# Kernel tuning notes

Measured on AMD Instinct MI355X. Metric: run time of the kernel, lower is better.

The kernel has to match this reference:

```python
import jax, jax.numpy as jnp
import numpy as np

B, SQ, D = 1, 2048, 1024          # batch, seq, hidden
H, DH = 16, 64                    # heads, head dim
NC = 4096                         # intermediate_size (num_class of LSH layer)
K, L = 8, 16                      # hash funcs per table, num tables
NBUCKETS = 2 ** K
TPP = 1024                        # num_tokens_per_pass
S = 1024                          # fixed LSH sample budget per chunk
P = 64                            # pos/neg set size for triplet loss
MARGIN = 0.5
EPS = 1e-12


def setup_inputs() -> dict:
    key = jax.random.key(0)
    ks = jax.random.split(key, 12)
    def n(k, shape, s=0.02):
        return jax.random.normal(k, shape, dtype=jnp.float32) * s
    return {
        "hidden_states": jax.random.normal(ks[0], (B, SQ, D), dtype=jnp.float32),
        "attention_mask": jnp.ones((B, SQ), jnp.float32),
        "ln1_g": jnp.ones((D,), jnp.float32), "ln1_b": jnp.zeros((D,), jnp.float32),
        "Wq": n(ks[1], (D, D)), "bq": jnp.zeros((D,), jnp.float32),
        "Wk": n(ks[2], (D, D)), "bk": jnp.zeros((D,), jnp.float32),
        "Wv": n(ks[3], (D, D)), "bv": jnp.zeros((D,), jnp.float32),
        "Wo": n(ks[4], (D, D)), "bo": jnp.zeros((D,), jnp.float32),
        "ln2_g": jnp.ones((D,), jnp.float32), "ln2_b": jnp.zeros((D,), jnp.float32),
        "W1": n(ks[5], (NC, D), 0.03), "b1": jnp.zeros((NC,), jnp.float32),
        "Whash": jax.random.normal(ks[6], (L, K, D), dtype=jnp.float32),
        "W2": n(ks[7], (NC, D), 0.0156), "b2": jnp.zeros((D,), jnp.float32),
    }


def _layernorm(x, g, b):
    m = x.mean(-1, keepdims=True)
    v = x.var(-1, keepdims=True)
    return (x - m) / jnp.sqrt(v + EPS) * g + b


def _forward(hidden_states, attention_mask, ln1_g, ln1_b, Wq, bq, Wk, bk, Wv, bv,
             Wo, bo, ln2_g, ln2_b, W1, b1, Whash, W2, b2):
    # ---------------- Attention (pre-LN, residual) ----------------
    x = _layernorm(hidden_states, ln1_g, ln1_b)
    def heads(w, bb):
        y = jnp.einsum('bsd,ed->bse', x, w) + bb
        return y.reshape(B, SQ, H, DH).transpose(0, 2, 1, 3)  # [B,H,S,DH]
    q, k, v = heads(Wq, bq), heads(Wk, bk), heads(Wv, bv)
    scale = DH ** 0.25                              # sqrt(sqrt(head_size))
    mask = -1000.0 * (1.0 - attention_mask)[:, None, None, :]
    scores = jnp.einsum('bhqd,bhkd->bhqk', q / scale, k / scale) + mask
    probs = jax.nn.softmax(scores, axis=-1)
    ctx = jnp.einsum('bhqk,bhkd->bhqd', probs, v)
    ctx = ctx.transpose(0, 2, 1, 3).reshape(B, SQ, D)
    attn_out = jnp.einsum('bsd,ed->bse', ctx, Wo) + bo + hidden_states

    # ---------------- SlideFFN: LSH-routed sparse FFN ----------------
    flat = attn_out.reshape(B * SQ, D)
    normed = _layernorm(flat, ln2_g, ln2_b)
    pow2 = (2 ** jnp.arange(K)).astype(jnp.int32)
    # rehash(): SimHash codes of all NC first-layer neurons, per table. [L, NC]
    code_n = (((jnp.einsum('lkd,nd->lnk', Whash, W1) > 0).astype(jnp.int32)) * pow2).sum(-1)

    def chunk_fn(h):                                 # h: [TPP, D]
        proj_t = jnp.einsum('lkd,td->ltk', Whash, h)              # [L,T,K]
        code_t = (((proj_t > 0).astype(jnp.int32)) * pow2).sum(-1)  # [L,T]
        # bucket histogram of token codes per table
        hist = jax.vmap(lambda c: jnp.zeros(NBUCKETS, jnp.float32).at[c].add(1.0))(code_t)
        # collision score per neuron: tokens sharing its bucket, summed over tables
        score = jnp.take_along_axis(hist, code_n, axis=1).sum(0)   # [NC]
        _, sids = jax.lax.top_k(score, S)                          # fixed sample budget
        w1s, b1s = W1[sids], b1[sids]                              # gather sampled rows
        logits = h @ w1s.T + b1s                                   # [T,S] sample_logits
        acts = jax.nn.gelu(logits, approximate=False)
        out = acts @ W2[sids] + b2                                 # [T,D]
        # triplet loss: hash agreement should track logit ranking
        proj_ns = jnp.einsum('lkd,sd->lsk', Whash, w1s)
        agree = jnp.einsum('ltk,lsk->ts', jnp.tanh(proj_t), jnp.tanh(proj_ns)) / (L * K)
        pos_idx = jax.lax.top_k(logits, P)[1]
        neg_idx = jax.lax.top_k(-logits, P)[1]
        a_pos = jnp.take_along_axis(agree, pos_idx, axis=1).mean(-1)
        a_neg = jnp.take_along_axis(agree, neg_idx, axis=1).mean(-1)
        triplet = jax.nn.relu(a_neg - a_pos + MARGIN).mean()
        return out, triplet

    C = (B * SQ) // TPP
    outs, trips = jax.vmap(chunk_fn)(normed.reshape(C, TPP, D))
    ffn_out = outs.reshape(B, SQ, D)
    layer_output = ffn_out + attn_out
    return layer_output, trips.mean()


def reference(hidden_states, attention_mask, ln1_g, ln1_b, Wq, bq, Wk, bk, Wv, bv,
              Wo, bo, ln2_g, ln2_b, W1, b1, Whash, W2, b2):
    return _forward(hidden_states, attention_mask, ln1_g, ln1_b, Wq, bq, Wk, bk,
                    Wv, bv, Wo, bo, ln2_g, ln2_b, W1, b1, Whash, W2, b2)
```

## Files before the change

### kernel.cpp

```cpp
#include <hip/hip_runtime.h>
#include <hip/hip_bf16.h>
#include <math.h>

typedef __hip_bfloat16 bf16;
__device__ __forceinline__ float b2f(bf16 x) { return __bfloat162float(x); }
__device__ __forceinline__ unsigned fkey(float f) {
    unsigned u = __float_as_uint(f);
    return (u & 0x80000000u) ? ~u : (u | 0x80000000u);
}

#define LN_EPS 1e-12f
#define NEG_INF (-3.0e38f)

__global__ __launch_bounds__(256)
void copy_int_kernel(const int* __restrict__ src, int* __restrict__ dst, int n)
{
    int i = blockIdx.x * 256 + threadIdx.x;
    if (i < n) dst[i] = src[i];
}

__global__ __launch_bounds__(256)
void ln_kernel(const float* __restrict__ in, const float* __restrict__ g,
               const float* __restrict__ b, float* __restrict__ out)
{
    const int D = 1024;
    int row = blockIdx.x, tid = threadIdx.x;
    size_t base = (size_t)row * D + tid * 4;
    float x[4];
    #pragma unroll
    for (int i = 0; i < 4; ++i) x[i] = in[base + i];
    double s  = (double)x[0] + x[1] + x[2] + x[3];
    double sq = (double)x[0]*x[0] + (double)x[1]*x[1] + (double)x[2]*x[2] + (double)x[3]*x[3];
    __shared__ double rs[256], rq[256];
    rs[tid] = s; rq[tid] = sq;
    __syncthreads();
    for (int o = 128; o > 0; o >>= 1) {
        if (tid < o) { rs[tid] += rs[tid + o]; rq[tid] += rq[tid + o]; }
        __syncthreads();
    }
    double mean = rs[0] * (1.0 / D);
    double var  = rq[0] * (1.0 / D) - mean * mean;
    double inv  = rsqrt(var + (double)LN_EPS);
    #pragma unroll
    for (int i = 0; i < 4; ++i) {
        int col = tid * 4 + i;
        out[base + i] = (float)(((double)x[i] - mean) * inv * (double)g[col] + (double)b[col]);
    }
}

#define BM 64
#define BN 64
#define BK 16
template<typename ACC>
__global__ __launch_bounds__(256)
void gemm_nt_t(const float* __restrict__ A, int lda,
               const float* __restrict__ B, int ldb,
               const int* __restrict__ gatherB,
               const float* __restrict__ bias,
               const float* __restrict__ residual,
               void* __restrict__ out_, int oBf, int ldc, int mode,
               int M, int N, int Kd)
{
    __shared__ __align__(16) float As[BK][BM + 4];
    __shared__ __align__(16) float Bs[BK][BN + 4];
    int tid = threadIdx.x;
    int bm = blockIdx.y * BM, bn = blockIdx.x * BN;
    int lm  = tid >> 2;
    int lk4 = (tid & 3) * 4;
    int tm = (tid >> 4) * 4, tn = (tid & 15) * 4;
    ACC acc[4][4] = {};
    for (int k0 = 0; k0 < Kd; k0 += BK) {
        {
            const float* p = A + (size_t)(bm + lm) * lda + k0 + lk4;
            #pragma unroll
            for (int i = 0; i < 4; ++i) As[lk4 + i][lm] = p[i];
        }
        {
            int r = bn + lm;
            if (gatherB) r = gatherB[r] & 4095;
            const float* p = B + (size_t)r * ldb + k0 + lk4;
            #pragma unroll
            for (int i = 0; i < 4; ++i) Bs[lk4 + i][lm] = p[i];
        }
        __syncthreads();
        #pragma unroll
        for (int k = 0; k < BK; ++k) {
            float4 av = *(const float4*)&As[k][tm];
            float4 bw = *(const float4*)&Bs[k][tn];
            float avx[4] = {av.x, av.y, av.z, av.w};
            float bwx[4] = {bw.x, bw.y, bw.z, bw.w};
            #pragma unroll
            for (int i = 0; i < 4; ++i)
                #pragma unroll
                for (int j = 0; j < 4; ++j)
                    acc[i][j] += (ACC)avx[i] * (ACC)bwx[j];
        }
        __syncthreads();
    }
    #pragma unroll
    for (int i = 0; i < 4; ++i) {
        int m = bm + tm + i;
        #pragma unroll
        for (int j = 0; j < 4; ++j) {
            int n = bn + tn + j;
            ACC v = acc[i][j];
            if (bias) { int bi2 = gatherB ? (gatherB[n] & 4095) : n; v += (ACC)bias[bi2]; }
            if (residual) v += (ACC)residual[(size_t)m * ldc + n];
            size_t idx;
            if (mode == 0)      idx = (size_t)m * ldc + n;
            else if (mode == 1) idx = (size_t)(n >> 6) * ((size_t)M * 64) + (size_t)m * 64 + (n & 63);
            else                idx = (size_t)(n >> 3) * ((size_t)M * 8) + (size_t)m * 8 + (n & 7);
            if (oBf) ((bf16*)out_)[idx] = __float2bfloat16((float)v);
            else     ((float*)out_)[idx] = (float)v;
        }
    }
}

__global__ __launch_bounds__(256)
void qkv_kernel(const float* __restrict__ A,
                const float* __restrict__ Wq, const float* __restrict__ Wk, const float* __restrict__ Wv,
                const float* __restrict__ bq, const float* __restrict__ bk, const float* __restrict__ bv,
                float* __restrict__ qo, float* __restrict__ ko, float* __restrict__ vo)
{
    const int lda = 1024, ldb = 1024, Kd = 1024, M = 2048;
    const float* B    = (blockIdx.z == 0) ? Wq : (blockIdx.z == 1) ? Wk : Wv;
    const float* bias = (blockIdx.z == 0) ? bq : (blockIdx.z == 1) ? bk : bv;
    float* out        = (blockIdx.z == 0) ? qo : (blockIdx.z == 1) ? ko : vo;
    __shared__ __align__(16) float As[BK][BM + 4];
    __shared__ __align__(16) float Bs[BK][BN + 4];
    int tid = threadIdx.x;
    int bm = blockIdx.y * BM, bn = blockIdx.x * BN;
    int lm  = tid >> 2;
    int lk4 = (tid & 3) * 4;
    int tm = (tid >> 4) * 4, tn = (tid & 15) * 4;
    float acc[4][4] = {};
    for (int k0 = 0; k0 < Kd; k0 += BK) {
        {
            const float* p = A + (size_t)(bm + lm) * lda + k0 + lk4;
            #pragma unroll
            for (int i = 0; i < 4; ++i) As[lk4 + i][lm] = p[i];
        }
        {
            const float* p = B + (size_t)(bn + lm) * ldb + k0 + lk4;
            #pragma unroll
            for (int i = 0; i < 4; ++i) Bs[lk4 + i][lm] = p[i];
        }
        __syncthreads();
        #pragma unroll
        for (int k = 0; k < BK; ++k) {
            float4 av = *(const float4*)&As[k][tm];
            float4 bw = *(const float4*)&Bs[k][tn];
            float avx[4] = {av.x, av.y, av.z, av.w};
            float bwx[4] = {bw.x, bw.y, bw.z, bw.w};
            #pragma unroll
            for (int i = 0; i < 4; ++i)
                #pragma unroll
                for (int j = 0; j < 4; ++j)
                    acc[i][j] += avx[i] * bwx[j];
        }
        __syncthreads();
    }
    #pragma unroll
    for (int i = 0; i < 4; ++i) {
        int m = bm + tm + i;
        #pragma unroll
        for (int j = 0; j < 4; ++j) {
            int n = bn + tn + j;
            float v = acc[i][j] + bias[n];
            size_t idx = (size_t)(n >> 6) * ((size_t)M * 64) + (size_t)m * 64 + (n & 63);
            out[idx] = v;
        }
    }
}

__global__ __launch_bounds__(256)
void logits_kernel(const float* __restrict__ normed, const float* __restrict__ W1,
                   const int* __restrict__ sids, const float* __restrict__ b1,
                   bf16* __restrict__ logits)
{
    const int lda = 1024, ldb = 1024, ldc = 1024, Kd = 1024;
    size_t chOff = (size_t)blockIdx.z * 1048576;
    const float* A = normed + chOff;
    const int* gk = sids + blockIdx.z * 1024;
    bf16* out = logits + chOff;
    __shared__ __align__(16) float As[BK][BM + 4];
    __shared__ __align__(16) float Bs[BK][BN + 4];
    int tid = threadIdx.x;
    int bm = blockIdx.y * BM, bn = blockIdx.x * BN;
    int lm  = tid >> 2;
    int lk4 = (tid & 3) * 4;
    int tm = (tid >> 4) * 4, tn = (tid & 15) * 4;
    float acc[4][4] = {};
    for (int k0 = 0; k0 < Kd; k0 += BK) {
        {
            const float* p = A + (size_t)(bm + lm) * lda + k0 + lk4;
            #pragma unroll
            for (int i = 0; i < 4; ++i) As[lk4 + i][lm] = p[i];
        }
        {
            int r = gk[bn + lm] & 4095;
            const float* p = W1 + (size_t)r * ldb + k0 + lk4;
            #pragma unroll
            for (int i = 0; i < 4; ++i) Bs[lk4 + i][lm] = p[i];
        }
        __syncthreads();
        #pragma unroll
        for (int k = 0; k < BK; ++k) {
            float4 av = *(const float4*)&As[k][tm];
            float4 bw = *(const float4*)&Bs[k][tn];
            float avx[4] = {av.x, av.y, av.z, av.w};
            float bwx[4] = {bw.x, bw.y, bw.z, bw.w};
            #pragma unroll
            for (int i = 0; i < 4; ++i)
                #pragma unroll
                for (int j = 0; j < 4; ++j)
                    acc[i][j] += avx[i] * bwx[j];
        }
        __syncthreads();
    }
    #pragma unroll
    for (int i = 0; i < 4; ++i) {
        int m = bm + tm + i;
        #pragma unroll
        for (int j = 0; j < 4; ++j) {
            int n = bn + tn + j;
            float v = acc[i][j] + b1[gk[n] & 4095];
            out[(size_t)m * ldc + n] = __float2bfloat16(v);
        }
    }
}

__global__ __launch_bounds__(256)
void out_kernel(const bf16* __restrict__ logits, const float* __restrict__ W2,
                const int* __restrict__ sids, const float* __restrict__ b2w,
                const float* __restrict__ attnO, float* __restrict__ out)
{
    const int lda = 1024, ldb = 1024, ldc = 1024, Kd = 1024;
    size_t chOff = (size_t)blockIdx.z * 1048576;
    const bf16* A = logits + chOff;
    const int* gk = sids + blockIdx.z * 1024;
    const float* residual = attnO + chOff;
    __shared__ __align__(16) float As[BK][BM + 4];
    __shared__ __align__(16) float Bs[BK][BN + 4];
    int tid = threadIdx.x;
    int bm = blockIdx.y * BM, bn = blockIdx.x * BN;
    int lm  = tid >> 2;
    int lk4 = (tid & 3) * 4;
    int bkr = tid >> 4;
    int bn4 = (tid & 15) * 4;
    int tm = (tid >> 4) * 4, tn = (tid & 15) * 4;
    float acc[4][4] = {};
    for (int k0 = 0; k0 < Kd; k0 += BK) {
        {
            const bf16* p = A + (size_t)(bm + lm) * lda + k0 + lk4;
            #pragma unroll
            for (int i = 0; i < 4; ++i) {
                float x = b2f(p[i]);
                As[lk4 + i][lm] = 0.5f * x * (1.0f + erff(x * 0.70710678118654752f));
            }
        }
        {
            int r = gk[k0 + bkr] & 4095;
            const float* q = W2 + (size_t)r * ldb + bn + bn4;
            #pragma unroll
            for (int i = 0; i < 4; ++i) Bs[bkr][bn4 + i] = q[i];
        }
        __syncthreads();
        #pragma unroll
        for (int k = 0; k < BK; ++k) {
            float4 av = *(const float4*)&As[k][tm];
            float4 bw = *(const float4*)&Bs[k][tn];
            float avx[4] = {av.x, av.y, av.z, av.w};
            float bwx[4] = {bw.x, bw.y, bw.z, bw.w};
            #pragma unroll
            for (int i = 0; i < 4; ++i)
                #pragma unroll
                for (int j = 0; j < 4; ++j)
                    acc[i][j] += avx[i] * bwx[j];
        }
        __syncthreads();
    }
    #pragma unroll
    for (int i = 0; i < 4; ++i) {
        int m = bm + tm + i;
        #pragma unroll
        for (int j = 0; j < 4; ++j) {
            int n = bn + tn + j;
            float v = acc[i][j] + b2w[n] + residual[(size_t)m * ldc + n];
            out[chOff + (size_t)m * ldc + n] = v;
        }
    }
}

__global__ __launch_bounds__(256)
void flash_kernel(const float* __restrict__ q, const float* __restrict__ k,
                  const float* __restrict__ v, const float* __restrict__ amask,
                  float* __restrict__ ctx, int hbase)
{
    int qt = blockIdx.x, hl = blockIdx.y, tid = threadIdx.x;
    int ty = tid >> 4, tx = tid & 15;
    int r0 = ty * 2;
    __shared__ __align__(16) float Qs[32][76];
    __shared__ __align__(16) float KVs[64][76];
    __shared__ __align__(16) float St[32][76];
    __shared__ float lrow[32], msk[64];
    const float* qh = q + (size_t)hl * 131072 + (size_t)qt * 2048;
    #pragma unroll
    for (int rep = 0; rep < 2; ++rep) {
        int lin = rep * 1024 + tid * 4;
        int r = lin >> 6, c = lin & 63;
        float4 u = *(const float4*)(qh + r * 64 + c);
        Qs[r][c] = u.x; Qs[r][c+1] = u.y; Qs[r][c+2] = u.z; Qs[r][c+3] = u.w;
    }
    if (tid < 32) lrow[tid] = 0.0f;
    float o0[4] = {}, o1[4] = {};
    for (int kt = 0; kt < 32; ++kt) {
        const float* kh = k + (size_t)hl * 131072 + (size_t)kt * 4096;
        const float* vh = v + (size_t)hl * 131072 + (size_t)kt * 4096;
        #pragma unroll
        for (int rep = 0; rep < 4; ++rep) {
            int lin = rep * 1024 + tid * 4;
            int r = lin >> 6, c = lin & 63;
            float4 u = *(const float4*)(kh + r * 64 + c);
            KVs[r][c] = u.x; KVs[r][c+1] = u.y; KVs[r][c+2] = u.z; KVs[r][c+3] = u.w;
        }
        if (tid < 64) msk[tid] = 1000.0f * (1.0f - amask[kt * 64 + tid]);
        __syncthreads();
        float sc0[4] = {}, sc1[4] = {};
        #pragma unroll 4
        for (int d = 0; d < 64; d += 4) {
            float4 q0 = *(const float4*)&Qs[r0][d];
            float4 q1 = *(const float4*)&Qs[r0 + 1][d];
            #pragma unroll
            for (int j = 0; j < 4; ++j) {
                float4 kv = *(const float4*)&KVs[tx + 16 * j][d];
                sc0[j] += q0.x * kv.x + q0.y * kv.y + q0.z * kv.z + q0.w * kv.w;
                sc1[j] += q1.x * kv.x + q1.y * kv.y + q1.z * kv.z + q1.w * kv.w;
            }
        }
        __syncthreads();
        float sum0 = 0.0f, sum1 = 0.0f;
        #pragma unroll
        for (int j = 0; j < 4; ++j) {
            float p0 = expf(sc0[j] * 0.125f - msk[tx + 16 * j]);
            float p1 = expf(sc1[j] * 0.125f - msk[tx + 16 * j]);
            St[r0][tx + 16 * j] = p0; St[r0 + 1][tx + 16 * j] = p1;
            sum0 += p0; sum1 += p1;
        }
        #pragma unroll
        for (int off = 1; off < 16; off <<= 1) {
            sum0 += __shfl_xor(sum0, off, 16);
            sum1 += __shfl_xor(sum1, off, 16);
        }
        if (tx == 0) { lrow[r0] += sum0; lrow[r0 + 1] += sum1; }
        #pragma unroll
        for (int rep = 0; rep < 4; ++rep) {
            int lin = rep * 1024 + tid * 4;
            int r = lin >> 6, c = lin & 63;
            float4 w = *(const float4*)(vh + r * 64 + c);
            KVs[r][c] = w.x; KVs[r][c+1] = w.y; KVs[r][c+2] = w.z; KVs[r][c+3] = w.w;
        }
        __syncthreads();
        for (int j2 = 0; j2 < 64; j2 += 4) {
            float4 p0v = *(const float4*)&St[r0][j2];
            float4 p1v = *(const float4*)&St[r0 + 1][j2];
            float p0a[4] = {p0v.x, p0v.y, p0v.z, p0v.w};
            float p1a[4] = {p1v.x, p1v.y, p1v.z, p1v.w};
            #pragma unroll
            for (int e = 0; e < 4; ++e) {
                float4 vv = *(const float4*)&KVs[j2 + e][tx * 4];
                o0[0] += p0a[e] * vv.x; o0[1] += p0a[e] * vv.y; o0[2] += p0a[e] * vv.z; o0[3] += p0a[e] * vv.w;
                o1[0] += p1a[e] * vv.x; o1[1] += p1a[e] * vv.y; o1[2] += p1a[e] * vv.z; o1[3] += p1a[e] * vv.w;
            }
        }
        __syncthreads();
    }
    float inv0 = 1.0f / lrow[r0], inv1 = 1.0f / lrow[r0 + 1];
    size_t base0 = (size_t)(qt * 32 + r0) * 1024 + (hbase + hl) * 64 + tx * 4;
    size_t base1 = base0 + 1024;
    #pragma unroll
    for (int j = 0; j < 4; ++j) {
        ctx[base0 + j] = o0[j] * inv0;
        ctx[base1 + j] = o1[j] * inv1;
    }
}

__global__ __launch_bounds__(256)
void code_n_kernel(const float* __restrict__ projn, int* __restrict__ code_n,
                   int* __restrict__ zero_base)
{
    int i = blockIdx.x * 256 + threadIdx.x;
    const float* p = projn + (size_t)i * 8;
    int code = 0;
    #pragma unroll
    for (int k = 0; k < 8; ++k) code |= ((int)(p[k] > 0.0f)) << k;
    code_n[i] = code;
    if (i < 49156) zero_base[i] = 0;
}

__global__ __launch_bounds__(256)
void code_t_kernel(float* __restrict__ pt, int* __restrict__ code_t)
{
    int i = blockIdx.x * 256 + threadIdx.x;
    int t = i >> 4, l = i & 15;
    float* p = pt + (size_t)t * 128 + l * 8;
    int code = 0;
    #pragma unroll
    for (int k = 0; k < 8; ++k) {
        float v = p[k];
        code |= ((int)(v > 0.0f)) << k;
        p[k] = tanhf(v);
    }
    code_t[l * 2048 + t] = code;
}

__global__ __launch_bounds__(256)
void hist_kernel(const int* __restrict__ code_t, int* __restrict__ hist)
{
    int i = blockIdx.x * 256 + threadIdx.x;
    int c = i >> 14, l = (i >> 10) & 15, t = i & 1023;
    int code = code_t[l * 2048 + c * 1024 + t] & 255;
    atomicAdd(&hist[(c * 16 + l) * 256 + code], 1);
}

__global__ __launch_bounds__(256)
void score_kernel(const int* __restrict__ hist, const int* __restrict__ code_n,
                  int* __restrict__ score, int* __restrict__ shist)
{
    int i = blockIdx.x * 256 + threadIdx.x;
    int c = i >> 12, n = i & 4095;
    int s = 0;
    #pragma unroll
    for (int l = 0; l < 16; ++l) s += hist[(c * 16 + l) * 256 + (code_n[l * 4096 + n] & 255)];
    if (s < 0) s = 0; if (s > 16384) s = 16384;
    score[c * 4096 + n] = s;
    atomicAdd(&shist[c * 16385 + s], 1);
}

__global__ __launch_bounds__(256)
void select_kernel(const int* __restrict__ shist, int* __restrict__ selmeta)
{
    int c = blockIdx.x, tid = threadIdx.x;
    const int* bins = shist + c * 16385;
    __shared__ int psum[256];
    int s = 0;
    for (int i = 0; i < 64; ++i) s += bins[tid * 64 + i];
    if (tid == 255) s += bins[16384];
    psum[tid] = s;
    __syncthreads();
    if (tid == 0) {
        int cum = 0, sstar = 0, cntge = 0;
        for (int t = 255; t >= 0; --t) {
            if (cum + psum[t] >= 1024) {
                int hi = (t == 255) ? 16384 : t * 64 + 63;
                for (int b = hi; b >= t * 64; --b) {
                    cum += bins[b];
                    if (cum >= 1024) { sstar = b; cntge = cum; break; }
                }
                break;
            }
            cum += psum[t];
        }
        selmeta[c * 2]     = sstar;
        selmeta[c * 2 + 1] = 1024 - (cntge - bins[sstar]);
    }
}

__global__ __launch_bounds__(256)
void build_sids_kernel(const int* __restrict__ score, const int* __restrict__ selmeta,
                       int* __restrict__ sids)
{
    int c = blockIdx.x, tid = threadIdx.x;
    const int* sc2 = score + c * 4096;
    int sstar = selmeta[c * 2], need_eq = selmeta[c * 2 + 1];
    __shared__ int scan[256];
    int base = tid * 16;
    int mysc[16];
    int eqc = 0;
    #pragma unroll
    for (int i = 0; i < 16; ++i) { mysc[i] = sc2[base + i]; eqc += (mysc[i] == sstar); }
    scan[tid] = eqc; __syncthreads();
    for (int o = 1; o < 256; o <<= 1) {
        int v = (tid >= o) ? scan[tid - o] : 0;
        __syncthreads();
        scan[tid] += v;
        __syncthreads();
    }
    int eqr = scan[tid] - eqc;
    __syncthreads();
    int selc = 0; unsigned flags = 0;
    #pragma unroll
    for (int i = 0; i < 16; ++i) {
        bool sel = false;
        if (mysc[i] > sstar) sel = true;
        else if (mysc[i] == sstar) { sel = (eqr < need_eq); eqr++; }
        if (sel) { flags |= (1u << i); selc++; }
    }
    scan[tid] = selc; __syncthreads();
    for (int o = 1; o < 256; o <<= 1) {
        int v = (tid >= o) ? scan[tid - o] : 0;
        __syncthreads();
        scan[tid] += v;
        __syncthreads();
    }
    int pos = scan[tid] - selc;
    #pragma unroll
    for (int i = 0; i < 16; ++i)
        if (flags & (1u << i)) { if (pos < 1024) sids[c * 1024 + pos] = base + i; pos++; }
}

__global__ __launch_bounds__(256)
void tanhpn_kernel(const float* __restrict__ projn, const int* __restrict__ sids,
                   float* __restrict__ tanhpn)
{
    int i = blockIdx.x * 256 + threadIdx.x;
    int c = i >> 17;
    int r = i & 131071;
    int s = r >> 7, j = r & 127;
    int l = j >> 3, k = j & 7;
    int n = sids[c * 1024 + s] & 4095;
    tanhpn[(size_t)c * 131072 + (size_t)s * 128 + j] = tanhf(projn[(size_t)l * 32768 + (size_t)n * 8 + k]);
}

__global__ __launch_bounds__(256)
void topk_kernel(const bf16* __restrict__ logits, const float* __restrict__ tanhpt,
                 const float* __restrict__ tanhpn, float* __restrict__ trip)
{
    int t = blockIdx.x;
    int c = t >> 10, tid = threadIdx.x;
    __shared__ float agr[1024];
    __shared__ float qrow[128];
    __shared__ int hist[256];
    __shared__ int scan[256];
    __shared__ float red[256];
    __shared__ int chosen_s, gsel_s;
    if (tid < 128) qrow[tid] = tanhpt[(size_t)t * 128 + tid];
    __syncthreads();
    for (int s = tid; s < 1024; s += 256) {
        const float* pn = tanhpn + ((size_t)c * 1024 + s) * 128;
        float acc = 0.0f;
        #pragma unroll 8
        for (int d = 0; d < 128; ++d) acc += qrow[d] * pn[d];
        agr[s] = acc * (1.0f / 128.0f);
    }
    const bf16* lrow = logits + (size_t)t * 1024;
    float v[4];
    #pragma unroll
    for (int j = 0; j < 4; ++j) v[j] = b2f(lrow[4 * tid + j]);
    __syncthreads();
    float mres[2];
    for (int p = 0; p < 2; ++p) {
        unsigned key[4];
        #pragma unroll
        for (int j = 0; j < 4; ++j) key[j] = fkey(p ? -v[j] : v[j]);
        unsigned prefix = 0;
        int gsel = 0;
        for (int pass = 0; pass < 4; ++pass) {
            int shift = 24 - 8 * pass;
            hist[tid] = 0;
            __syncthreads();
            #pragma unroll
            for (int j = 0; j < 4; ++j) {
                bool match = (pass == 0) || ((key[j] >> (shift + 8)) == prefix);
                if (match) atomicAdd(&hist[(key[j] >> shift) & 255], 1);
            }
            __syncthreads();
            if (tid == 0) {
                int need = 64 - gsel;
                int acc = 0, b = 255;
                for (; b >= 0; --b) {
                    int h = hist[b];
                    if (acc + h >= need) break;
                    acc += h;
                }
                chosen_s = b;
                gsel_s = gsel + acc;
            }
            __syncthreads();
            prefix = (prefix << 8) | (unsigned)chosen_s;
            gsel = gsel_s;
        }
        unsigned kstar = prefix;
        int need_eq = 64 - gsel;
        float asum = 0.0f;
        int eqc = 0;
        #pragma unroll
        for (int j = 0; j < 4; ++j) {
            if (key[j] > kstar) asum += agr[4 * tid + j];
            else if (key[j] == kstar) eqc++;
        }
        scan[tid] = eqc;
        __syncthreads();
        for (int o = 1; o < 256; o <<= 1) {
            int val = (tid >= o) ? scan[tid - o] : 0;
            __syncthreads();
            scan[tid] += val;
            __syncthreads();
        }
        int eqr = scan[tid] - eqc;
        #pragma unroll
        for (int j = 0; j < 4; ++j) {
            if (key[j] == kstar) { if (eqr < need_eq) asum += agr[4 * tid + j]; eqr++; }
        }
        red[tid] = asum;
        __syncthreads();
        for (int o = 128; o > 0; o >>= 1) {
            if (tid < o) red[tid] += red[tid + o];
            __syncthreads();
        }
        mres[p] = red[0] * (1.0f / 64.0f);
        __syncthreads();
    }
    if (tid == 0) {
        float r = mres[1] - mres[0] + 0.5f;
        trip[t] = r > 0.0f ? r : 0.0f;
    }
}

__global__ __launch_bounds__(256)
void trip_mean_kernel(const float* __restrict__ trip, float* __restrict__ out)
{
    int tid = threadIdx.x;
    float s = 0.0f;
    for (int i = tid; i < 2048; i += 256) s += trip[i];
    __shared__ float rs[256];
    rs[tid] = s; __syncthreads();
    for (int o = 128; o > 0; o >>= 1) { if (tid < o) rs[tid] += rs[tid + o]; __syncthreads(); }
    if (tid == 0) out[2097152] = rs[0] * (1.0f / 2048.0f);
}

extern "C" void kernel_launch(void* const* d_in, const int* in_sizes, int n_in,
                              void* d_out, int out_size, void* d_ws, size_t ws_size,
                              hipStream_t stream)
{
    const float* hidden = (const float*)d_in[0];
    const float* amask  = (const float*)d_in[1];
    const float* ln1g   = (const float*)d_in[2];
    const float* ln1b   = (const float*)d_in[3];
    const float* Wq     = (const float*)d_in[4];
    const float* bq     = (const float*)d_in[5];
    const float* Wk     = (const float*)d_in[6];
    const float* bk     = (const float*)d_in[7];
    const float* Wv     = (const float*)d_in[8];
    const float* bv     = (const float*)d_in[9];
    const float* Wo     = (const float*)d_in[10];
    const float* bo     = (const float*)d_in[11];
    const float* ln2g   = (const float*)d_in[12];
    const float* ln2b   = (const float*)d_in[13];
    const float* W1     = (const float*)d_in[14];
    const float* b1     = (const float*)d_in[15];
    const float* Whash  = (const float*)d_in[16];
    const float* W2     = (const float*)d_in[17];
    const float* b2w    = (const float*)d_in[18];
    float* out = (float*)d_out;
    float* ws  = (float*)d_ws;
    const size_t MB = 1024 * 1024;
    if (ws_size < 20 * MB) return;

    float* xln    = ws;
    float* qg     = ws + 2097152;
    float* kg     = ws + 3145728;
    float* vg     = ws + 4194304;
    float* attnO  = ws + 2097152;
    float* normed = ws;
    bf16*  logits = (bf16*)(ws + 4194304);
    int*   sids_ws = (int*)ws;

    float* ctx    = out;
    float* projn  = out;
    float* tanhpt = out + 524288;
    float* tanhpn = out + 786432;
    int*   dints  = (int*)out + 1048576;
    int*   code_n = dints;
    int*   code_t = dints + 65536;
    int*   hist   = dints + 98304;
    int*   score  = dints + 106496;
    int*   shist  = dints + 114688;
    int*   selmeta= dints + 147460;
    int*   sids   = dints + 147464;
    float* trip   = (float*)(dints + 149512);

    ln_kernel<<<2048, 256, 0, stream>>>(hidden, ln1g, ln1b, xln);
    for (int g = 0; g < 2; ++g) {
        const size_t wOff = (size_t)g * 512 * 1024;
        qkv_kernel<<<dim3(8, 32, 3), 256, 0, stream>>>(xln, Wq + wOff, Wk + wOff, Wv + wOff,
                                                       bq + g * 512, bk + g * 512, bv + g * 512,
                                                       qg, kg, vg);
        flash_kernel<<<dim3(64, 8), 256, 0, stream>>>(qg, kg, vg, amask, ctx, g * 8);
    }
    gemm_nt_t<float><<<dim3(16, 32), 256, 0, stream>>>(ctx, 1024, Wo, 1024, nullptr, bo, hidden, attnO, 0, 1024, 0, 2048, 1024, 1024);

    ln_kernel<<<2048, 256, 0, stream>>>(attnO, ln2g, ln2b, normed);
    gemm_nt_t<double><<<dim3(2, 64), 256, 0, stream>>>(W1, 1024, Whash, 1024, nullptr, nullptr, nullptr, projn, 0, 0, 3, 4096, 128, 1024);
    code_n_kernel<<<256, 256, 0, stream>>>(projn, code_n, hist);
    gemm_nt_t<double><<<dim3(2, 32), 256, 0, stream>>>(normed, 1024, Whash, 1024, nullptr, nullptr, nullptr, tanhpt, 0, 128, 0, 2048, 128, 1024);
    code_t_kernel<<<128, 256, 0, stream>>>(tanhpt, code_t);
    hist_kernel<<<128, 256, 0, stream>>>(code_t, hist);
    score_kernel<<<32, 256, 0, stream>>>(hist, code_n, score, shist);
    select_kernel<<<2, 256, 0, stream>>>(shist, selmeta);
    build_sids_kernel<<<2, 256, 0, stream>>>(score, selmeta, sids);
    tanhpn_kernel<<<1024, 256, 0, stream>>>(projn, sids, tanhpn);

    logits_kernel<<<dim3(16, 16, 2), 256, 0, stream>>>(normed, W1, sids, b1, logits);

    topk_kernel<<<2048, 256, 0, stream>>>(logits, tanhpt, tanhpn, trip);
    trip_mean_kernel<<<1, 256, 0, stream>>>(trip, out);

    copy_int_kernel<<<8, 256, 0, stream>>>(sids, sids_ws, 2048);
    out_kernel<<<dim3(16, 16, 2), 256, 0, stream>>>(logits, W2, sids_ws, b2w, attnO, out);
}
```

Baseline: 1.501 ms.

## Enlarge GEMM and flash-attention register tiles to 8x4 and 64-row blocks

Moves the QKV, output-projection, logits and FFN-out GEMMs from 64x64 tiles with a 4x4 per-thread accumulator to 128x64 tiles with an 8x4 accumulator and vectorized float4/ushort4 global loads. The flash-attention kernel now handles 64 query rows per block instead of 32, with each thread computing a 4x4 block of scores and outputs. The aim is more arithmetic per shared-memory and global load and fewer blocks. The cost is more registers and fewer blocks in flight, which can lower occupancy.

```diff
diff --git a/kernel.cpp b/kernel.cpp
--- a/kernel.cpp
+++ b/kernel.cpp
@@ -117,6 +117,75 @@
 }
 
 __global__ __launch_bounds__(256)
+void gemm_f32_big(const float* __restrict__ A, int lda,
+                  const float* __restrict__ B, int ldb,
+                  const int* __restrict__ gatherB,
+                  const float* __restrict__ bias,
+                  const float* __restrict__ residual,
+                  void* __restrict__ out_, int oBf, int ldc, int mode,
+                  int M, int Kd,
+                  size_t aStride, size_t oStride, int gStride)
+{
+    __shared__ __align__(16) float As[16][132];
+    __shared__ __align__(16) float Bs[16][68];
+    int tid = threadIdx.x;
+    const float* Ab = A + (size_t)blockIdx.z * aStride;
+    const int* gb = gatherB ? gatherB + blockIdx.z * gStride : nullptr;
+    size_t oOff = (size_t)blockIdx.z * oStride;
+    int bm = blockIdx.y * 128, bn = blockIdx.x * 64;
+    int lmA = tid >> 1, kA = (tid & 1) * 8;
+    int lmB = tid >> 2, kB = (tid & 3) * 4;
+    int rB = bn + lmB; if (gb) rB = gb[rB] & 4095;
+    int tm = (tid >> 4) * 8, tn = (tid & 15) * 4;
+    float acc[8][4] = {};
+    for (int k0 = 0; k0 < Kd; k0 += 16) {
+        {
+            const float* pa = Ab + (size_t)(bm + lmA) * lda + k0 + kA;
+            float4 a0 = *(const float4*)pa;
+            float4 a1 = *(const float4*)(pa + 4);
+            As[kA+0][lmA]=a0.x; As[kA+1][lmA]=a0.y; As[kA+2][lmA]=a0.z; As[kA+3][lmA]=a0.w;
+            As[kA+4][lmA]=a1.x; As[kA+5][lmA]=a1.y; As[kA+6][lmA]=a1.z; As[kA+7][lmA]=a1.w;
+        }
+        {
+            const float* pb = B + (size_t)rB * ldb + k0 + kB;
+            float4 b0 = *(const float4*)pb;
+            Bs[kB+0][lmB]=b0.x; Bs[kB+1][lmB]=b0.y; Bs[kB+2][lmB]=b0.z; Bs[kB+3][lmB]=b0.w;
+        }
+        __syncthreads();
+        #pragma unroll
+        for (int k = 0; k < 16; ++k) {
+            float4 alo = *(const float4*)&As[k][tm];
+            float4 ahi = *(const float4*)&As[k][tm + 4];
+            float4 bw  = *(const float4*)&Bs[k][tn];
+            float avx[8] = {alo.x, alo.y, alo.z, alo.w, ahi.x, ahi.y, ahi.z, ahi.w};
+            float bwx[4] = {bw.x, bw.y, bw.z, bw.w};
+            #pragma unroll
+            for (int i = 0; i < 8; ++i)
+                #pragma unroll
+                for (int j = 0; j < 4; ++j)
+                    acc[i][j] += avx[i] * bwx[j];
+        }
+        __syncthreads();
+    }
+    #pragma unroll
+    for (int i = 0; i < 8; ++i) {
+        int m = bm + tm + i;
+        #pragma unroll
+        for (int j = 0; j < 4; ++j) {
+            int n = bn + tn + j;
+            float v = acc[i][j];
+            if (bias) { int bi2 = gb ? (gb[n] & 4095) : n; v += bias[bi2]; }
+            if (residual) v += residual[(size_t)m * ldc + n];
+            size_t idx;
+            if (mode == 0) idx = (size_t)m * ldc + n;
+            else           idx = (size_t)(n >> 6) * ((size_t)M * 64) + (size_t)m * 64 + (n & 63);
+            if (oBf) ((bf16*)out_)[oOff + idx] = __float2bfloat16(v);
+            else     ((float*)out_)[oOff + idx] = v;
+        }
+    }
+}
+
+__global__ __launch_bounds__(256)
 void qkv_kernel(const float* __restrict__ A,
                 const float* __restrict__ Wq, const float* __restrict__ Wk, const float* __restrict__ Wv,
                 const float* __restrict__ bq, const float* __restrict__ bk, const float* __restrict__ bv,
@@ -126,34 +195,37 @@
     const float* B    = (blockIdx.z == 0) ? Wq : (blockIdx.z == 1) ? Wk : Wv;
     const float* bias = (blockIdx.z == 0) ? bq : (blockIdx.z == 1) ? bk : bv;
     float* out        = (blockIdx.z == 0) ? qo : (blockIdx.z == 1) ? ko : vo;
-    __shared__ __align__(16) float As[BK][BM + 4];
-    __shared__ __align__(16) float Bs[BK][BN + 4];
+    __shared__ __align__(16) float As[16][132];
+    __shared__ __align__(16) float Bs[16][68];
     int tid = threadIdx.x;
-    int bm = blockIdx.y * BM, bn = blockIdx.x * BN;
-    int lm  = tid >> 2;
-    int lk4 = (tid & 3) * 4;
-    int tm = (tid >> 4) * 4, tn = (tid & 15) * 4;
-    float acc[4][4] = {};
-    for (int k0 = 0; k0 < Kd; k0 += BK) {
+    int bm = blockIdx.y * 128, bn = blockIdx.x * 64;
+    int lmA = tid >> 1, kA = (tid & 1) * 8;
+    int lmB = tid >> 2, kB = (tid & 3) * 4;
+    int tm = (tid >> 4) * 8, tn = (tid & 15) * 4;
+    float acc[8][4] = {};
+    for (int k0 = 0; k0 < Kd; k0 += 16) {
         {
-            const float* p = A + (size_t)(bm + lm) * lda + k0 + lk4;
-            #pragma unroll
-            for (int i = 0; i < 4; ++i) As[lk4 + i][lm] = p[i];
+            const float* pa = A + (size_t)(bm + lmA) * lda + k0 + kA;
+            float4 a0 = *(const float4*)pa;
+            float4 a1 = *(const float4*)(pa + 4);
+            As[kA+0][lmA]=a0.x; As[kA+1][lmA]=a0.y; As[kA+2][lmA]=a0.z; As[kA+3][lmA]=a0.w;
+            As[kA+4][lmA]=a1.x; As[kA+5][lmA]=a1.y; As[kA+6][lmA]=a1.z; As[kA+7][lmA]=a1.w;
         }
         {
-            const float* p = B + (size_t)(bn + lm) * ldb + k0 + lk4;
-            #pragma unroll
-            for (int i = 0; i < 4; ++i) Bs[lk4 + i][lm] = p[i];
-        }
-        __syncthreads();
-        #pragma unroll
-        for (int k = 0; k < BK; ++k) {
-            float4 av = *(const float4*)&As[k][tm];
-            float4 bw = *(const float4*)&Bs[k][tn];
-            float avx[4] = {av.x, av.y, av.z, av.w};
+            const float* pb = B + (size_t)(bn + lmB) * ldb + k0 + kB;
+            float4 b0 = *(const float4*)pb;
+            Bs[kB+0][lmB]=b0.x; Bs[kB+1][lmB]=b0.y; Bs[kB+2][lmB]=b0.z; Bs[kB+3][lmB]=b0.w;
+        }
+        __syncthreads();
+        #pragma unroll
+        for (int k = 0; k < 16; ++k) {
+            float4 alo = *(const float4*)&As[k][tm];
+            float4 ahi = *(const float4*)&As[k][tm + 4];
+            float4 bw  = *(const float4*)&Bs[k][tn];
+            float avx[8] = {alo.x, alo.y, alo.z, alo.w, ahi.x, ahi.y, ahi.z, ahi.w};
             float bwx[4] = {bw.x, bw.y, bw.z, bw.w};
             #pragma unroll
-            for (int i = 0; i < 4; ++i)
+            for (int i = 0; i < 8; ++i)
                 #pragma unroll
                 for (int j = 0; j < 4; ++j)
                     acc[i][j] += avx[i] * bwx[j];
@@ -161,7 +233,7 @@
         __syncthreads();
     }
     #pragma unroll
-    for (int i = 0; i < 4; ++i) {
+    for (int i = 0; i < 8; ++i) {
         int m = bm + tm + i;
         #pragma unroll
         for (int j = 0; j < 4; ++j) {
@@ -174,63 +246,6 @@
 }
 
 __global__ __launch_bounds__(256)
-void logits_kernel(const float* __restrict__ normed, const float* __restrict__ W1,
-                   const int* __restrict__ sids, const float* __restrict__ b1,
-                   bf16* __restrict__ logits)
-{
-    const int lda = 1024, ldb = 1024, ldc = 1024, Kd = 1024;
-    size_t chOff = (size_t)blockIdx.z * 1048576;
-    const float* A = normed + chOff;
-    const int* gk = sids + blockIdx.z * 1024;
-    bf16* out = logits + chOff;
-    __shared__ __align__(16) float As[BK][BM + 4];
-    __shared__ __align__(16) float Bs[BK][BN + 4];
-    int tid = threadIdx.x;
-    int bm = blockIdx.y * BM, bn = blockIdx.x * BN;
-    int lm  = tid >> 2;
-    int lk4 = (tid & 3) * 4;
-    int tm = (tid >> 4) * 4, tn = (tid & 15) * 4;
-    float acc[4][4] = {};
-    for (int k0 = 0; k0 < Kd; k0 += BK) {
-        {
-            const float* p = A + (size_t)(bm + lm) * lda + k0 + lk4;
-            #pragma unroll
-            for (int i = 0; i < 4; ++i) As[lk4 + i][lm] = p[i];
-        }
-        {
-            int r = gk[bn + lm] & 4095;
-            const float* p = W1 + (size_t)r * ldb + k0 + lk4;
-            #pragma unroll
-            for (int i = 0; i < 4; ++i) Bs[lk4 + i][lm] = p[i];
-        }
-        __syncthreads();
-        #pragma unroll
-        for (int k = 0; k < BK; ++k) {
-            float4 av = *(const float4*)&As[k][tm];
-            float4 bw = *(const float4*)&Bs[k][tn];
-            float avx[4] = {av.x, av.y, av.z, av.w};
-            float bwx[4] = {bw.x, bw.y, bw.z, bw.w};
-            #pragma unroll
-            for (int i = 0; i < 4; ++i)
-                #pragma unroll
-                for (int j = 0; j < 4; ++j)
-                    acc[i][j] += avx[i] * bwx[j];
-        }
-        __syncthreads();
-    }
-    #pragma unroll
-    for (int i = 0; i < 4; ++i) {
-        int m = bm + tm + i;
-        #pragma unroll
-        for (int j = 0; j < 4; ++j) {
-            int n = bn + tn + j;
-            float v = acc[i][j] + b1[gk[n] & 4095];
-            out[(size_t)m * ldc + n] = __float2bfloat16(v);
-        }
-    }
-}
-
-__global__ __launch_bounds__(256)
 void out_kernel(const bf16* __restrict__ logits, const float* __restrict__ W2,
                 const int* __restrict__ sids, const float* __restrict__ b2w,
                 const float* __restrict__ attnO, float* __restrict__ out)
@@ -240,40 +255,42 @@
     const bf16* A = logits + chOff;
     const int* gk = sids + blockIdx.z * 1024;
     const float* residual = attnO + chOff;
-    __shared__ __align__(16) float As[BK][BM + 4];
-    __shared__ __align__(16) float Bs[BK][BN + 4];
+    __shared__ __align__(16) float As[16][132];
+    __shared__ __align__(16) float Bs[16][68];
     int tid = threadIdx.x;
-    int bm = blockIdx.y * BM, bn = blockIdx.x * BN;
-    int lm  = tid >> 2;
-    int lk4 = (tid & 3) * 4;
-    int bkr = tid >> 4;
-    int bn4 = (tid & 15) * 4;
-    int tm = (tid >> 4) * 4, tn = (tid & 15) * 4;
-    float acc[4][4] = {};
-    for (int k0 = 0; k0 < Kd; k0 += BK) {
+    int bm = blockIdx.y * 128, bn = blockIdx.x * 64;
+    int lmA = tid >> 1, kA = (tid & 1) * 8;
+    int kRow = tid >> 4, nOff = (tid & 15) * 4;
+    int tm = (tid >> 4) * 8, tn = (tid & 15) * 4;
+    float acc[8][4] = {};
+    for (int k0 = 0; k0 < Kd; k0 += 16) {
         {
-            const bf16* p = A + (size_t)(bm + lm) * lda + k0 + lk4;
-            #pragma unroll
-            for (int i = 0; i < 4; ++i) {
-                float x = b2f(p[i]);
-                As[lk4 + i][lm] = 0.5f * x * (1.0f + erff(x * 0.70710678118654752f));
+            const unsigned short* pa = (const unsigned short*)A + (size_t)(bm + lmA) * lda + k0 + kA;
+            ushort4 u0 = *(const ushort4*)pa;
+            ushort4 u1 = *(const ushort4*)(pa + 4);
+            unsigned short us[8] = {u0.x, u0.y, u0.z, u0.w, u1.x, u1.y, u1.z, u1.w};
+            #pragma unroll
+            for (int i = 0; i < 8; ++i) {
+                union { unsigned u; float f; } w; w.u = ((unsigned)us[i]) << 16;
+                float x = w.f;
+                As[kA + i][lmA] = 0.5f * x * (1.0f + erff(x * 0.70710678118654752f));
             }
         }
         {
-            int r = gk[k0 + bkr] & 4095;
-            const float* q = W2 + (size_t)r * ldb + bn + bn4;
-            #pragma unroll
-            for (int i = 0; i < 4; ++i) Bs[bkr][bn4 + i] = q[i];
-        }
-        __syncthreads();
-        #pragma unroll
-        for (int k = 0; k < BK; ++k) {
-            float4 av = *(const float4*)&As[k][tm];
-            float4 bw = *(const float4*)&Bs[k][tn];
-            float avx[4] = {av.x, av.y, av.z, av.w};
+            int r = gk[k0 + kRow] & 4095;
+            float4 b0 = *(const float4*)(W2 + (size_t)r * ldb + bn + nOff);
+            *(float4*)&Bs[kRow][nOff] = b0;
+        }
+        __syncthreads();
+        #pragma unroll
+        for (int k = 0; k < 16; ++k) {
+            float4 alo = *(const float4*)&As[k][tm];
+            float4 ahi = *(const float4*)&As[k][tm + 4];
+            float4 bw  = *(const float4*)&Bs[k][tn];
+            float avx[8] = {alo.x, alo.y, alo.z, alo.w, ahi.x, ahi.y, ahi.z, ahi.w};
             float bwx[4] = {bw.x, bw.y, bw.z, bw.w};
             #pragma unroll
-            for (int i = 0; i < 4; ++i)
+            for (int i = 0; i < 8; ++i)
                 #pragma unroll
                 for (int j = 0; j < 4; ++j)
                     acc[i][j] += avx[i] * bwx[j];
@@ -281,7 +298,7 @@
         __syncthreads();
     }
     #pragma unroll
-    for (int i = 0; i < 4; ++i) {
+    for (int i = 0; i < 8; ++i) {
         int m = bm + tm + i;
         #pragma unroll
         for (int j = 0; j < 4; ++j) {
@@ -299,21 +316,20 @@
 {
     int qt = blockIdx.x, hl = blockIdx.y, tid = threadIdx.x;
     int ty = tid >> 4, tx = tid & 15;
-    int r0 = ty * 2;
-    __shared__ __align__(16) float Qs[32][76];
+    __shared__ __align__(16) float Qs[64][76];
     __shared__ __align__(16) float KVs[64][76];
-    __shared__ __align__(16) float St[32][76];
-    __shared__ float lrow[32], msk[64];
-    const float* qh = q + (size_t)hl * 131072 + (size_t)qt * 2048;
-    #pragma unroll
-    for (int rep = 0; rep < 2; ++rep) {
+    __shared__ __align__(16) float St[64][76];
+    __shared__ float lrow[64], msk[64];
+    const float* qh = q + (size_t)hl * 131072 + (size_t)qt * 4096;
+    #pragma unroll
+    for (int rep = 0; rep < 4; ++rep) {
         int lin = rep * 1024 + tid * 4;
         int r = lin >> 6, c = lin & 63;
         float4 u = *(const float4*)(qh + r * 64 + c);
         Qs[r][c] = u.x; Qs[r][c+1] = u.y; Qs[r][c+2] = u.z; Qs[r][c+3] = u.w;
     }
-    if (tid < 32) lrow[tid] = 0.0f;
-    float o0[4] = {}, o1[4] = {};
+    if (tid < 64) lrow[tid] = 0.0f;
+    float o[4][4] = {};
     for (int kt = 0; kt < 32; ++kt) {
         const float* kh = k + (size_t)hl * 131072 + (size_t)kt * 4096;
         const float* vh = v + (size_t)hl * 131072 + (size_t)kt * 4096;
@@ -326,33 +342,40 @@
         }
         if (tid < 64) msk[tid] = 1000.0f * (1.0f - amask[kt * 64 + tid]);
         __syncthreads();
-        float sc0[4] = {}, sc1[4] = {};
+        float sc[4][4] = {};
         #pragma unroll 4
         for (int d = 0; d < 64; d += 4) {
-            float4 q0 = *(const float4*)&Qs[r0][d];
-            float4 q1 = *(const float4*)&Qs[r0 + 1][d];
+            float4 qv[4];
+            #pragma unroll
+            for (int i = 0; i < 4; ++i) qv[i] = *(const float4*)&Qs[ty + 16 * i][d];
             #pragma unroll
             for (int j = 0; j < 4; ++j) {
                 float4 kv = *(const float4*)&KVs[tx + 16 * j][d];
-                sc0[j] += q0.x * kv.x + q0.y * kv.y + q0.z * kv.z + q0.w * kv.w;
-                sc1[j] += q1.x * kv.x + q1.y * kv.y + q1.z * kv.z + q1.w * kv.w;
+                #pragma unroll
+                for (int i = 0; i < 4; ++i)
+                    sc[i][j] += qv[i].x * kv.x + qv[i].y * kv.y + qv[i].z * kv.z + qv[i].w * kv.w;
             }
         }
         __syncthreads();
-        float sum0 = 0.0f, sum1 = 0.0f;
-        #pragma unroll
-        for (int j = 0; j < 4; ++j) {
-            float p0 = expf(sc0[j] * 0.125f - msk[tx + 16 * j]);
-            float p1 = expf(sc1[j] * 0.125f - msk[tx + 16 * j]);
-            St[r0][tx + 16 * j] = p0; St[r0 + 1][tx + 16 * j] = p1;
-            sum0 += p0; sum1 += p1;
+        float sum[4] = {};
+        #pragma unroll
+        for (int i = 0; i < 4; ++i) {
+            #pragma unroll
+            for (int j = 0; j < 4; ++j) {
+                float p = expf(sc[i][j] * 0.125f - msk[tx + 16 * j]);
+                St[ty + 16 * i][tx + 16 * j] = p;
+                sum[i] += p;
+            }
         }
         #pragma unroll
         for (int off = 1; off < 16; off <<= 1) {
-            sum0 += __shfl_xor(sum0, off, 16);
-            sum1 += __shfl_xor(sum1, off, 16);
-        }
-        if (tx == 0) { lrow[r0] += sum0; lrow[r0 + 1] += sum1; }
+            #pragma unroll
+            for (int i = 0; i < 4; ++i) sum[i] += __shfl_xor(sum[i], off, 16);
+        }
+        if (tx == 0) {
+            #pragma unroll
+            for (int i = 0; i < 4; ++i) lrow[ty + 16 * i] += sum[i];
+        }
         #pragma unroll
         for (int rep = 0; rep < 4; ++rep) {
             int lin = rep * 1024 + tid * 4;
@@ -362,26 +385,31 @@
         }
         __syncthreads();
         for (int j2 = 0; j2 < 64; j2 += 4) {
-            float4 p0v = *(const float4*)&St[r0][j2];
-            float4 p1v = *(const float4*)&St[r0 + 1][j2];
-            float p0a[4] = {p0v.x, p0v.y, p0v.z, p0v.w};
-            float p1a[4] = {p1v.x, p1v.y, p1v.z, p1v.w};
+            float4 pv[4];
+            #pragma unroll
+            for (int i = 0; i < 4; ++i) pv[i] = *(const float4*)&St[ty + 16 * i][j2];
+            float pa[4][4];
+            #pragma unroll
+            for (int i = 0; i < 4; ++i) { pa[i][0]=pv[i].x; pa[i][1]=pv[i].y; pa[i][2]=pv[i].z; pa[i][3]=pv[i].w; }
             #pragma unroll
             for (int e = 0; e < 4; ++e) {
                 float4 vv = *(const float4*)&KVs[j2 + e][tx * 4];
-                o0[0] += p0a[e] * vv.x; o0[1] += p0a[e] * vv.y; o0[2] += p0a[e] * vv.z; o0[3] += p0a[e] * vv.w;
-                o1[0] += p1a[e] * vv.x; o1[1] += p1a[e] * vv.y; o1[2] += p1a[e] * vv.z; o1[3] += p1a[e] * vv.w;
+                #pragma unroll
+                for (int i = 0; i < 4; ++i) {
+                    o[i][0] += pa[i][e] * vv.x; o[i][1] += pa[i][e] * vv.y;
+                    o[i][2] += pa[i][e] * vv.z; o[i][3] += pa[i][e] * vv.w;
+                }
             }
         }
         __syncthreads();
     }
-    float inv0 = 1.0f / lrow[r0], inv1 = 1.0f / lrow[r0 + 1];
-    size_t base0 = (size_t)(qt * 32 + r0) * 1024 + (hbase + hl) * 64 + tx * 4;
-    size_t base1 = base0 + 1024;
-    #pragma unroll
-    for (int j = 0; j < 4; ++j) {
-        ctx[base0 + j] = o0[j] * inv0;
-        ctx[base1 + j] = o1[j] * inv1;
+    #pragma unroll
+    for (int i = 0; i < 4; ++i) {
+        int row = ty + 16 * i;
+        float inv = 1.0f / lrow[row];
+        size_t base = (size_t)(qt * 64 + row) * 1024 + (hbase + hl) * 64 + tx * 4;
+        #pragma unroll
+        for (int j = 0; j < 4; ++j) ctx[base + j] = o[i][j] * inv;
     }
 }
 
@@ -683,12 +711,13 @@
     ln_kernel<<<2048, 256, 0, stream>>>(hidden, ln1g, ln1b, xln);
     for (int g = 0; g < 2; ++g) {
         const size_t wOff = (size_t)g * 512 * 1024;
-        qkv_kernel<<<dim3(8, 32, 3), 256, 0, stream>>>(xln, Wq + wOff, Wk + wOff, Wv + wOff,
+        qkv_kernel<<<dim3(8, 16, 3), 256, 0, stream>>>(xln, Wq + wOff, Wk + wOff, Wv + wOff,
                                                        bq + g * 512, bk + g * 512, bv + g * 512,
                                                        qg, kg, vg);
-        flash_kernel<<<dim3(64, 8), 256, 0, stream>>>(qg, kg, vg, amask, ctx, g * 8);
-    }
-    gemm_nt_t<float><<<dim3(16, 32), 256, 0, stream>>>(ctx, 1024, Wo, 1024, nullptr, bo, hidden, attnO, 0, 1024, 0, 2048, 1024, 1024);
+        flash_kernel<<<dim3(32, 8), 256, 0, stream>>>(qg, kg, vg, amask, ctx, g * 8);
+    }
+    gemm_f32_big<<<dim3(16, 16, 1), 256, 0, stream>>>(ctx, 1024, Wo, 1024, nullptr, bo, hidden,
+                                                      attnO, 0, 1024, 0, 2048, 1024, 0, 0, 0);
 
     ln_kernel<<<2048, 256, 0, stream>>>(attnO, ln2g, ln2b, normed);
     gemm_nt_t<double><<<dim3(2, 64), 256, 0, stream>>>(W1, 1024, Whash, 1024, nullptr, nullptr, nullptr, projn, 0, 0, 3, 4096, 128, 1024);
@@ -701,11 +730,13 @@
     build_sids_kernel<<<2, 256, 0, stream>>>(score, selmeta, sids);
     tanhpn_kernel<<<1024, 256, 0, stream>>>(projn, sids, tanhpn);
 
-    logits_kernel<<<dim3(16, 16, 2), 256, 0, stream>>>(normed, W1, sids, b1, logits);
+    gemm_f32_big<<<dim3(16, 8, 2), 256, 0, stream>>>(normed, 1024, W1, 1024, sids, b1, nullptr,
+                                                     logits, 1, 1024, 0, 2048, 1024,
+                                                     1048576, 1048576, 1024);
 
     topk_kernel<<<2048, 256, 0, stream>>>(logits, tanhpt, tanhpn, trip);
     trip_mean_kernel<<<1, 256, 0, stream>>>(trip, out);
 
     copy_int_kernel<<<8, 256, 0, stream>>>(sids, sids_ws, 2048);
-    out_kernel<<<dim3(16, 16, 2), 256, 0, stream>>>(logits, W2, sids_ws, b2w, attnO, out);
-}
+    out_kernel<<<dim3(16, 8, 2), 256, 0, stream>>>(logits, W2, sids_ws, b2w, attnO, out);
+}
```

After: 1.634 ms. 8.8% more time.

## Prefetch next K/V tile into registers and split K/V shared buffers

Applied to the files above, without the earlier changes.

The flash attention kernel now keeps separate shared buffers for K and V. It loads the next K and V tiles from global memory into registers while the current tile is being computed, so global-load latency overlaps with the dot products and the exp work. Because V is staged together with K, one barrier per iteration goes away, and the shared stores now use float4. In exchange the kernel uses more shared memory and 32 more registers per thread, which may lower occupancy.

```diff
diff --git a/kernel.cpp b/kernel.cpp
--- a/kernel.cpp
+++ b/kernel.cpp
@@ -301,7 +301,8 @@
     int ty = tid >> 4, tx = tid & 15;
     int r0 = ty * 2;
     __shared__ __align__(16) float Qs[32][76];
-    __shared__ __align__(16) float KVs[64][76];
+    __shared__ __align__(16) float Ks[64][76];
+    __shared__ __align__(16) float Vs[64][76];
     __shared__ __align__(16) float St[32][76];
     __shared__ float lrow[32], msk[64];
     const float* qh = q + (size_t)hl * 131072 + (size_t)qt * 2048;
@@ -309,23 +310,39 @@
     for (int rep = 0; rep < 2; ++rep) {
         int lin = rep * 1024 + tid * 4;
         int r = lin >> 6, c = lin & 63;
-        float4 u = *(const float4*)(qh + r * 64 + c);
-        Qs[r][c] = u.x; Qs[r][c+1] = u.y; Qs[r][c+2] = u.z; Qs[r][c+3] = u.w;
+        *(float4*)&Qs[r][c] = *(const float4*)(qh + lin);
     }
     if (tid < 32) lrow[tid] = 0.0f;
+    const float* kh = k + (size_t)hl * 131072;
+    const float* vh = v + (size_t)hl * 131072;
+    float4 kf[4], vf[4];
+    #pragma unroll
+    for (int rep = 0; rep < 4; ++rep) {
+        int lin = rep * 1024 + tid * 4;
+        kf[rep] = *(const float4*)(kh + lin);
+        vf[rep] = *(const float4*)(vh + lin);
+    }
     float o0[4] = {}, o1[4] = {};
     for (int kt = 0; kt < 32; ++kt) {
-        const float* kh = k + (size_t)hl * 131072 + (size_t)kt * 4096;
-        const float* vh = v + (size_t)hl * 131072 + (size_t)kt * 4096;
         #pragma unroll
         for (int rep = 0; rep < 4; ++rep) {
             int lin = rep * 1024 + tid * 4;
             int r = lin >> 6, c = lin & 63;
-            float4 u = *(const float4*)(kh + r * 64 + c);
-            KVs[r][c] = u.x; KVs[r][c+1] = u.y; KVs[r][c+2] = u.z; KVs[r][c+3] = u.w;
+            *(float4*)&Ks[r][c] = kf[rep];
+            *(float4*)&Vs[r][c] = vf[rep];
         }
         if (tid < 64) msk[tid] = 1000.0f * (1.0f - amask[kt * 64 + tid]);
         __syncthreads();
+        if (kt < 31) {
+            const float* khn = k + (size_t)hl * 131072 + (size_t)(kt + 1) * 4096;
+            const float* vhn = v + (size_t)hl * 131072 + (size_t)(kt + 1) * 4096;
+            #pragma unroll
+            for (int rep = 0; rep < 4; ++rep) {
+                int lin = rep * 1024 + tid * 4;
+                kf[rep] = *(const float4*)(khn + lin);
+                vf[rep] = *(const float4*)(vhn + lin);
+            }
+        }
         float sc0[4] = {}, sc1[4] = {};
         #pragma unroll 4
         for (int d = 0; d < 64; d += 4) {
@@ -333,12 +350,11 @@
             float4 q1 = *(const float4*)&Qs[r0 + 1][d];
             #pragma unroll
             for (int j = 0; j < 4; ++j) {
-                float4 kv = *(const float4*)&KVs[tx + 16 * j][d];
+                float4 kv = *(const float4*)&Ks[tx + 16 * j][d];
                 sc0[j] += q0.x * kv.x + q0.y * kv.y + q0.z * kv.z + q0.w * kv.w;
                 sc1[j] += q1.x * kv.x + q1.y * kv.y + q1.z * kv.z + q1.w * kv.w;
             }
         }
-        __syncthreads();
         float sum0 = 0.0f, sum1 = 0.0f;
         #pragma unroll
         for (int j = 0; j < 4; ++j) {
@@ -353,13 +369,6 @@
             sum1 += __shfl_xor(sum1, off, 16);
         }
         if (tx == 0) { lrow[r0] += sum0; lrow[r0 + 1] += sum1; }
-        #pragma unroll
-        for (int rep = 0; rep < 4; ++rep) {
-            int lin = rep * 1024 + tid * 4;
-            int r = lin >> 6, c = lin & 63;
-            float4 w = *(const float4*)(vh + r * 64 + c);
-            KVs[r][c] = w.x; KVs[r][c+1] = w.y; KVs[r][c+2] = w.z; KVs[r][c+3] = w.w;
-        }
         __syncthreads();
         for (int j2 = 0; j2 < 64; j2 += 4) {
             float4 p0v = *(const float4*)&St[r0][j2];
@@ -368,7 +377,7 @@
             float p1a[4] = {p1v.x, p1v.y, p1v.z, p1v.w};
             #pragma unroll
             for (int e = 0; e < 4; ++e) {
-                float4 vv = *(const float4*)&KVs[j2 + e][tx * 4];
+                float4 vv = *(const float4*)&Vs[j2 + e][tx * 4];
                 o0[0] += p0a[e] * vv.x; o0[1] += p0a[e] * vv.y; o0[2] += p0a[e] * vv.z; o0[3] += p0a[e] * vv.w;
                 o1[0] += p1a[e] * vv.x; o1[1] += p1a[e] * vv.y; o1[2] += p1a[e] * vv.z; o1[3] += p1a[e] * vv.w;
             }
```

Result: no change. 1.486 ms (-1.0%).
